# Kernel optimization log

Hardware: AMD Instinct MI355X
Metric: run time of the kernel (lower is better)

Reference implementation:

```python
import jax, jax.numpy as jnp
import numpy as np

RADIUS = 2
MAXDISP = 192


def _lga(x, g, radius=RADIUS):
    """Local guided aggregation (GANet LGA).
    x: [B, D, H, W] cost volume. g: [B, 3*k*k, H, W] L1-normalized guidance.
    out[b,d,p] = sum_off g0[off,p]*x[d,p+off] + g1[off,p]*x[d-1,p+off] + g2[off,p]*x[d+1,p+off]
    """
    B, D, H, W = x.shape
    k = 2 * radius + 1
    g0, g1, g2 = jnp.split(g, 3, axis=1)  # each [B, k*k, H, W]
    pad_sp = ((0, 0), (0, 0), (radius, radius), (radius, radius))
    x_p = jnp.pad(x, pad_sp)
    # disparity-shifted volumes (zero padded at the ends)
    x_dm = jnp.pad(x, ((0, 0), (1, 0), (0, 0), (0, 0)))[:, :D]   # x[d-1]
    x_dp = jnp.pad(x, ((0, 0), (0, 1), (0, 0), (0, 0)))[:, 1:]   # x[d+1]
    xm_p = jnp.pad(x_dm, pad_sp)
    xp_p = jnp.pad(x_dp, pad_sp)
    out = jnp.zeros_like(x)
    idx = 0
    for i in range(k):
        for j in range(k):
            sl = (slice(None), slice(None), slice(i, i + H), slice(j, j + W))
            out = out + (x_p[sl] * g0[:, idx][:, None]
                         + xm_p[sl] * g1[:, idx][:, None]
                         + xp_p[sl] * g2[:, idx][:, None])
            idx += 1
    return out


def _forward(x, lg1, conv_w):
    B = x.shape[0]
    H8, W8 = x.shape[3] * 8, x.shape[4] * 8
    # conv32x1: 3x3x3 conv, 32 -> 1 channels, padding 1, no bias
    x = jax.lax.conv_general_dilated(
        x, conv_w, window_strides=(1, 1, 1), padding=[(1, 1)] * 3,
        dimension_numbers=("NCDHW", "OIDHW", "NCDHW"))  # [B,1,D,H/8,W/8]
    # trilinear upsample (align_corners=False / half-pixel centers)
    x = jax.image.resize(x, (B, 1, MAXDISP + 1, H8, W8), method="linear")
    x = jnp.squeeze(x, 1)  # [B, D+1, H, W]
    # L1-normalize guidance over channel dim (F.normalize p=1 dim=1)
    g = lg1 / jnp.maximum(jnp.sum(jnp.abs(lg1), axis=1, keepdims=True), 1e-12)
    # LGA2 = local guided aggregation applied twice with the same guidance
    x = _lga(x, g)
    x = _lga(x, g)
    # softmin over disparity, then L1 normalize over disparity
    p = jax.nn.softmax(-x, axis=1)
    p = p / jnp.maximum(jnp.sum(jnp.abs(p), axis=1, keepdims=True), 1e-12)
    disps = jnp.arange(MAXDISP + 1, dtype=p.dtype)
    return jnp.einsum("bdhw,d->bhw", p, disps)


def setup_inputs() -> dict:
    key = jax.random.key(0)
    k1, k2, k3 = jax.random.split(key, 3)
    x = jax.random.normal(k1, (1, 32, 49, 32, 64), dtype=jnp.float32)
    lg1 = jax.random.uniform(k2, (1, 75, 256, 512), dtype=jnp.float32)
    conv_w = jax.random.normal(k3, (1, 32, 3, 3, 3), dtype=jnp.float32) * 0.05
    return {"x": x, "lg1": lg1, "conv_w": conv_w}


def reference(x, lg1, conv_w):
    return _forward(x, lg1, conv_w)
```

## Files before the change

### kernel.cpp

```cpp
#include <hip/hip_runtime.h>
#include <hip/hip_bf16.h>

#define DIN 49
#define HIN 32
#define WIN 64
#define CIN 32
#define DOUT 193
#define HOUT 256
#define WOUT 512
#define NPIX (HOUT * WOUT)
#define NUPS (DOUT * NPIX)
#define NCONV (DIN * HIN * WIN)
#define DSPLIT 193
#define NZ 1
#define CGRP 8

#define ROWSTRIDE 33
#define PIXSTRIDE 12
#define SUWORDS 7920

typedef __attribute__((ext_vector_type(2))) float v2f;
typedef __attribute__((ext_vector_type(4))) float v4f;

__device__ __forceinline__ v2f pk_fma(v2f a, v2f b, v2f c) {
    v2f d;
    asm("v_pk_fma_f32 %0, %1, %2, %3" : "=v"(d) : "v"(a), "v"(b), "v"(c));
    return d;
}

__global__ void conv3d_kernel(const float* __restrict__ x,
                              const float* __restrict__ w,
                              float* __restrict__ partial) {
    __shared__ float ws[4 * 27];
    const int grp = blockIdx.y;
    for (int t = threadIdx.x; t < 4 * 27; t += blockDim.x)
        ws[t] = w[grp * (4 * 27) + t];
    __syncthreads();

    int idx4 = blockIdx.x * blockDim.x + threadIdx.x;
    int w4 = idx4 & 15;
    int t2 = idx4 >> 4;
    int hq = t2 & 31;
    int dq = t2 >> 5;
    int wq0 = w4 * 4;

    float acc0 = 0.f, acc1 = 0.f, acc2 = 0.f, acc3 = 0.f;
    const float* xg = x + (size_t)grp * 4 * NCONV;
#pragma unroll
    for (int cl = 0; cl < 4; ++cl) {
        const float* xb = xg + cl * NCONV;
        const float* wb = ws + cl * 27;
#pragma unroll
        for (int kd = 0; kd < 3; ++kd) {
            int zd = dq + kd - 1;
            if (zd < 0 || zd >= DIN) continue;
#pragma unroll
            for (int kh = 0; kh < 3; ++kh) {
                int zh = hq + kh - 1;
                if (zh < 0 || zh >= HIN) continue;
                const float* row = xb + (zd * HIN + zh) * WIN;
                float4 v = *(const float4*)(row + wq0);
                float xl = (wq0 > 0) ? row[wq0 - 1] : 0.f;
                float xr = (wq0 < WIN - 4) ? row[wq0 + 4] : 0.f;
                float w0 = wb[(kd * 3 + kh) * 3 + 0];
                float w1 = wb[(kd * 3 + kh) * 3 + 1];
                float w2 = wb[(kd * 3 + kh) * 3 + 2];
                acc0 = fmaf(w0, xl, acc0);
                acc0 = fmaf(w1, v.x, acc0);
                acc0 = fmaf(w2, v.y, acc0);
                acc1 = fmaf(w0, v.x, acc1);
                acc1 = fmaf(w1, v.y, acc1);
                acc1 = fmaf(w2, v.z, acc1);
                acc2 = fmaf(w0, v.y, acc2);
                acc2 = fmaf(w1, v.z, acc2);
                acc2 = fmaf(w2, v.w, acc2);
                acc3 = fmaf(w0, v.z, acc3);
                acc3 = fmaf(w1, v.w, acc3);
                acc3 = fmaf(w2, xr, acc3);
            }
        }
    }
    float4 o4 = make_float4(acc0, acc1, acc2, acc3);
    *(float4*)(partial + (size_t)grp * NCONV + (size_t)idx4 * 4) = o4;
}

__global__ void convfold_kernel(const float* __restrict__ partial,
                                float* __restrict__ c) {
    int idx = blockIdx.x * blockDim.x + threadIdx.x;
    float s = 0.f;
#pragma unroll
    for (int g = 0; g < CGRP; ++g) s += partial[(size_t)g * NCONV + idx];
    c[idx] = s;
}

__device__ __forceinline__ unsigned short bf16bits(float f) {
    __hip_bfloat16 h = __float2bfloat16(f);
    unsigned short b;
    __builtin_memcpy(&b, &h, 2);
    return b;
}

#define GW(idx)                                                  \
    __uint_as_float(((idx) & 1) ? (gp[(idx) >> 1] & 0xFFFF0000u) \
                                : (gp[(idx) >> 1] << 16))

#define TAP_PK(A0, A1, B0, B1, C0, g0, g1, g2)   \
    do {                                         \
        v2f g1b = {g1, g1};                      \
        v2f g2b = {g2, g2};                      \
        acc01 = pk_fma(g1b, A0, acc01);          \
        acc01 = pk_fma(g2b, A1, acc01);          \
        acc23 = pk_fma(g1b, A1, acc23);          \
        acc23 = pk_fma(g2b, B0, acc23);          \
        acc45 = pk_fma(g1b, B0, acc45);          \
        acc45 = pk_fma(g2b, B1, acc45);          \
        acc67 = pk_fma(g1b, B1, acc67);          \
        acc67 = pk_fma(g2b, C0, acc67);          \
        acc01.x = fmaf(g0, A0.y, acc01.x);       \
        acc01.y = fmaf(g0, A1.x, acc01.y);       \
        acc23.x = fmaf(g0, A1.y, acc23.x);       \
        acc23.y = fmaf(g0, B0.x, acc23.y);       \
        acc45.x = fmaf(g0, B0.y, acc45.x);       \
        acc45.y = fmaf(g0, B1.x, acc45.y);       \
        acc67.x = fmaf(g0, B1.y, acc67.x);       \
        acc67.y = fmaf(g0, C0.x, acc67.y);       \
    } while (0)

__device__ __forceinline__ void stageA1(const float* __restrict__ cvol,
                                        int tid, int h0p, int w0p, int dstart,
                                        unsigned (&aq0)[4], unsigned (&aq2)[2]) {
    aq2[0] = 0u;
    aq2[1] = 0u;
#pragma unroll
    for (int k = 0; k < 4; ++k) {
        const bool a = (k < 3) || (tid < 32);
        int j = tid + k * 256;
        int seg = j & 3;
        int rowjob = j >> 2;
        int dl = rowjob / 20;
        int r = rowjob - dl * 20;
        int gh = h0p - 2 + r;
        int gwb = w0p - 8 + seg * 8;
        int gd = dstart - 1 + dl;
        if (a && gd >= 0 && gd < DOUT && gh >= 0 && gh < HOUT && gwb >= 0 &&
            (gwb + 8) <= WOUT) {
            float fd = (gd + 0.5f) * (49.0f / 193.0f) - 0.5f;
            fd = fminf(fmaxf(fd, 0.f), (float)(DIN - 1));
            int d0c = min((int)fd, DIN - 2);
            float ad = fd - (float)d0c;
            float fh = (gh + 0.5f) * 0.125f - 0.5f;
            fh = fminf(fmaxf(fh, 0.f), (float)(HIN - 1));
            int h0c = min((int)fh, HIN - 2);
            float ah = fh - (float)h0c;
            int g = gwb >> 3;
            int cm1 = max(g - 1, 0);
            int cp1 = min(g + 1, WIN - 1);
            const float* p00 = cvol + (d0c * HIN + h0c) * WIN;
            const float* p01 = p00 + WIN;
            const float* p10 = p00 + HIN * WIN;
            const float* p11 = p10 + WIN;
            float q00, q01, q10, q11, a0, a1, a2;
            q00 = p00[cm1]; q01 = p01[cm1];
            q10 = p10[cm1]; q11 = p11[cm1];
            a0 = (q00 + ah * (q01 - q00)) * (1.f - ad) +
                 (q10 + ah * (q11 - q10)) * ad;
            q00 = p00[g]; q01 = p01[g];
            q10 = p10[g]; q11 = p11[g];
            a1 = (q00 + ah * (q01 - q00)) * (1.f - ad) +
                 (q10 + ah * (q11 - q10)) * ad;
            q00 = p00[cp1]; q01 = p01[cp1];
            q10 = p10[cp1]; q11 = p11[cp1];
            a2 = (q00 + ah * (q01 - q00)) * (1.f - ad) +
                 (q10 + ah * (q11 - q10)) * ad;
            aq0[k] = (unsigned)bf16bits(a0) | ((unsigned)bf16bits(a1) << 16);
            aq2[k >> 1] |= ((unsigned)bf16bits(a2)) << ((k & 1) * 16);
        } else {
            aq0[k] = 0u;
        }
    }
}

__device__ __forceinline__ void scat1(float* __restrict__ su, int tid,
                                      const unsigned (&aq0)[4],
                                      const unsigned (&aq2)[2]) {
#pragma unroll
    for (int k = 0; k < 4; ++k) {
        if (k < 3 || tid < 32) {
            int j = tid + k * 256;
            int seg = j & 3;
            int rowjob = j >> 2;
            int dl = rowjob / 20;
            int r = rowjob - dl * 20;
            int base = (r * ROWSTRIDE + seg * 8) * PIXSTRIDE + dl;
            float a0 = __uint_as_float(aq0[k] << 16);
            float a1 = __uint_as_float(aq0[k] & 0xFFFF0000u);
            float a2 = __uint_as_float((k & 1) ? (aq2[k >> 1] & 0xFFFF0000u)
                                               : (aq2[k >> 1] << 16));
            float d01 = a1 - a0, d12 = a2 - a1;
            su[base + 0 * PIXSTRIDE] = a0 + 0.5625f * d01;
            su[base + 1 * PIXSTRIDE] = a0 + 0.6875f * d01;
            su[base + 2 * PIXSTRIDE] = a0 + 0.8125f * d01;
            su[base + 3 * PIXSTRIDE] = a0 + 0.9375f * d01;
            su[base + 4 * PIXSTRIDE] = a1 + 0.0625f * d12;
            su[base + 5 * PIXSTRIDE] = a1 + 0.1875f * d12;
            su[base + 6 * PIXSTRIDE] = a1 + 0.3125f * d12;
            su[base + 7 * PIXSTRIDE] = a1 + 0.4375f * d12;
        }
    }
}

__device__ __forceinline__ void stageA2(const unsigned short* __restrict__ xus,
                                        int tid, int h0p, int w0p, int dstart,
                                        uint4 (&dat)[4]) {
#pragma unroll
    for (int k = 0; k < 4; ++k) {
        const bool a = (k < 3) || (tid < 32);
        int j = tid + k * 256;
        int seg = j & 3;
        int rowjob = j >> 2;
        int dl = rowjob / 20;
        int r = rowjob - dl * 20;
        int gh = h0p - 2 + r;
        int gwb = w0p - 8 + seg * 8;
        int gd = dstart - 1 + dl;
        uint4 v = make_uint4(0u, 0u, 0u, 0u);
        if (a && gd >= 0 && gd < DOUT && gh >= 0 && gh < HOUT && gwb >= 0 &&
            (gwb + 8) <= WOUT)
            v = *(const uint4*)(xus + (size_t)gd * NPIX + gh * WOUT + gwb);
        dat[k] = v;
    }
}

__device__ __forceinline__ void scat2(float* __restrict__ su, int tid,
                                      const uint4 (&dat)[4]) {
#pragma unroll
    for (int k = 0; k < 4; ++k) {
        if (k < 3 || tid < 32) {
            int j = tid + k * 256;
            int seg = j & 3;
            int rowjob = j >> 2;
            int dl = rowjob / 20;
            int r = rowjob - dl * 20;
            int base = (r * ROWSTRIDE + seg * 8) * PIXSTRIDE + dl;
            unsigned q;
            q = dat[k].x;
            su[base + 0 * PIXSTRIDE] = __uint_as_float(q << 16);
            su[base + 1 * PIXSTRIDE] = __uint_as_float(q & 0xFFFF0000u);
            q = dat[k].y;
            su[base + 2 * PIXSTRIDE] = __uint_as_float(q << 16);
            su[base + 3 * PIXSTRIDE] = __uint_as_float(q & 0xFFFF0000u);
            q = dat[k].z;
            su[base + 4 * PIXSTRIDE] = __uint_as_float(q << 16);
            su[base + 5 * PIXSTRIDE] = __uint_as_float(q & 0xFFFF0000u);
            q = dat[k].w;
            su[base + 6 * PIXSTRIDE] = __uint_as_float(q << 16);
            su[base + 7 * PIXSTRIDE] = __uint_as_float(q & 0xFFFF0000u);
        }
    }
}

__global__ __launch_bounds__(256)
__attribute__((amdgpu_num_vgpr(128))) void lga1_kernel(
    const float* __restrict__ cvol,
    const float* __restrict__ lg1,
    __hip_bfloat16* __restrict__ yout) {
    const int tid = threadIdx.x;
    const int tx = tid & 15;
    const int ty = tid >> 4;
    const int w0p = blockIdx.x * 16;
    const int h0p = blockIdx.y * 16;
    const int zb = 0;
    const int dend = DOUT;
    const int pix = (h0p + ty) * WOUT + (w0p + tx);

    __shared__ __align__(16) float su[2 * SUWORDS];

    unsigned aq0[4], aq2[2];
    stageA1(cvol, tid, h0p, w0p, zb, aq0, aq2);

    float asum = 0.f;
    unsigned gp[38];
#pragma unroll
    for (int p = 0; p < 38; ++p) {
        int c0 = 2 * p, c1 = 2 * p + 1;
        float w0 = lg1[c0 * NPIX + pix];
        float w1 = (c1 < 75) ? lg1[c1 * NPIX + pix] : 0.f;
        unsigned b0 = bf16bits(w0), b1 = bf16bits(w1);
        asum += fabsf(__uint_as_float(b0 << 16)) +
                fabsf(__uint_as_float(b1 << 16));
        gp[p] = b0 | (b1 << 16);
    }
    const float inv = 1.f / fmaxf(asum, 1e-12f);

    const int pbase = (ty * ROWSTRIDE + tx + 6) * PIXSTRIDE;
    __hip_bfloat16* ybase = yout + pix;

    scat1(su, tid, aq0, aq2);
    int pb = 0;
    for (int d0 = zb; d0 < dend; d0 += 8) {
        __syncthreads();
        const bool hn = (d0 + 8 < dend);
        if (hn) stageA1(cvol, tid, h0p, w0p, d0 + 8, aq0, aq2);

        const float* sw = su + pb * SUWORDS + pbase;
        v2f acc01 = {0.f, 0.f}, acc23 = {0.f, 0.f};
        v2f acc45 = {0.f, 0.f}, acc67 = {0.f, 0.f};
#pragma unroll
        for (int i = 0; i < 5; ++i) {
#pragma unroll
            for (int j = 0; j < 5; ++j) {
                const int t = i * 5 + j;
                const float* sp = sw + (i * ROWSTRIDE + j) * PIXSTRIDE;
                v4f va = *(const v4f*)sp;
                v4f vb = *(const v4f*)(sp + 4);
                v2f vc = *(const v2f*)(sp + 8);
                v2f A0 = va.xy, A1 = va.zw, B0 = vb.xy, B1 = vb.zw;
                const float g0 = GW(t);
                const float g1 = GW(25 + t);
                const float g2 = GW(50 + t);
                TAP_PK(A0, A1, B0, B1, vc, g0, g1, g2);
            }
        }

        if (hn) scat1(su + (pb ^ 1) * SUWORDS, tid, aq0, aq2);

        float acc[8] = {acc01.x, acc01.y, acc23.x, acc23.y,
                        acc45.x, acc45.y, acc67.x, acc67.y};
        if (d0 + 8 <= dend) {
#pragma unroll
            for (int dd = 0; dd < 8; ++dd)
                ybase[(size_t)(d0 + dd) * NPIX] =
                    __float2bfloat16(acc[dd] * inv);
        } else {
#pragma unroll
            for (int dd = 0; dd < 8; ++dd)
                if (d0 + dd < dend)
                    ybase[(size_t)(d0 + dd) * NPIX] =
                        __float2bfloat16(acc[dd] * inv);
        }
        pb ^= 1;
    }
}

__global__ __launch_bounds__(256)
__attribute__((amdgpu_num_vgpr(128))) void lga2_kernel(
    const __hip_bfloat16* __restrict__ xin,
    const float* __restrict__ lg1,
    float* __restrict__ out) {
    const int tid = threadIdx.x;
    const int tx = tid & 15;
    const int ty = tid >> 4;
    const int w0p = blockIdx.x * 16;
    const int h0p = blockIdx.y * 16;
    const int zb = 0;
    const int dend = DOUT;
    const int pix = (h0p + ty) * WOUT + (w0p + tx);
    const unsigned short* xus = (const unsigned short*)xin;

    __shared__ __align__(16) float su[2 * SUWORDS];

    uint4 dat[4];
    stageA2(xus, tid, h0p, w0p, zb, dat);

    float asum = 0.f;
    unsigned gp[38];
#pragma unroll
    for (int p = 0; p < 38; ++p) {
        int c0 = 2 * p, c1 = 2 * p + 1;
        float w0 = lg1[c0 * NPIX + pix];
        float w1 = (c1 < 75) ? lg1[c1 * NPIX + pix] : 0.f;
        unsigned b0 = bf16bits(w0), b1 = bf16bits(w1);
        asum += fabsf(__uint_as_float(b0 << 16)) +
                fabsf(__uint_as_float(b1 << 16));
        gp[p] = b0 | (b1 << 16);
    }
    const float inv = 1.f / fmaxf(asum, 1e-12f);

    const int pbase = (ty * ROWSTRIDE + tx + 6) * PIXSTRIDE;

    float m = -1e30f, l = 0.f, s_acc = 0.f;

    scat2(su, tid, dat);
    int pb = 0;
    for (int d0 = zb; d0 < dend; d0 += 8) {
        __syncthreads();
        const bool hn = (d0 + 8 < dend);
        if (hn) stageA2(xus, tid, h0p, w0p, d0 + 8, dat);

        const float* sw = su + pb * SUWORDS + pbase;
        v2f acc01 = {0.f, 0.f}, acc23 = {0.f, 0.f};
        v2f acc45 = {0.f, 0.f}, acc67 = {0.f, 0.f};
#pragma unroll
        for (int i = 0; i < 5; ++i) {
#pragma unroll
            for (int j = 0; j < 5; ++j) {
                const int t = i * 5 + j;
                const float* sp = sw + (i * ROWSTRIDE + j) * PIXSTRIDE;
                v4f va = *(const v4f*)sp;
                v4f vb = *(const v4f*)(sp + 4);
                v2f vc = *(const v2f*)(sp + 8);
                v2f A0 = va.xy, A1 = va.zw, B0 = vb.xy, B1 = vb.zw;
                const float g0 = GW(t);
                const float g1 = GW(25 + t);
                const float g2 = GW(50 + t);
                TAP_PK(A0, A1, B0, B1, vc, g0, g1, g2);
            }
        }

        if (hn) scat2(su + (pb ^ 1) * SUWORDS, tid, dat);

        float acc[8] = {acc01.x, acc01.y, acc23.x, acc23.y,
                        acc45.x, acc45.y, acc67.x, acc67.y};
        if (d0 + 8 <= dend) {
            float v0 = -acc[0] * inv, v1 = -acc[1] * inv;
            float v2 = -acc[2] * inv, v3 = -acc[3] * inv;
            float v4 = -acc[4] * inv, v5 = -acc[5] * inv;
            float v6 = -acc[6] * inv, v7 = -acc[7] * inv;
            float mx = fmaxf(fmaxf(fmaxf(v0, v1), fmaxf(v2, v3)),
                             fmaxf(fmaxf(v4, v5), fmaxf(v6, v7)));
            mx = fmaxf(mx, m);
            float sc = __expf(m - mx);
            float e0 = __expf(v0 - mx), e1 = __expf(v1 - mx);
            float e2 = __expf(v2 - mx), e3 = __expf(v3 - mx);
            float e4 = __expf(v4 - mx), e5 = __expf(v5 - mx);
            float e6 = __expf(v6 - mx), e7 = __expf(v7 - mx);
            l = l * sc + ((e0 + e1) + (e2 + e3)) + ((e4 + e5) + (e6 + e7));
            float fd0 = (float)d0;
            s_acc = s_acc * sc + e0 * fd0 + e1 * (fd0 + 1.f) +
                    e2 * (fd0 + 2.f) + e3 * (fd0 + 3.f) + e4 * (fd0 + 4.f) +
                    e5 * (fd0 + 5.f) + e6 * (fd0 + 6.f) + e7 * (fd0 + 7.f);
            m = mx;
        } else {
#pragma unroll
            for (int dd = 0; dd < 8; ++dd) {
                int d = d0 + dd;
                if (d < dend) {
                    float v = -acc[dd] * inv;
                    float mx = fmaxf(m, v);
                    float sc = __expf(m - mx);
                    float e = __expf(v - mx);
                    l = l * sc + e;
                    s_acc = s_acc * sc + e * (float)d;
                    m = mx;
                }
            }
        }
        pb ^= 1;
    }

    out[pix] = s_acc / l;
}
#undef GW

extern "C" void kernel_launch(void* const* d_in, const int* in_sizes, int n_in,
                              void* d_out, int out_size, void* d_ws,
                              size_t ws_size, hipStream_t stream) {
    const float* x = (const float*)d_in[0];
    const float* lg1 = (const float*)d_in[1];
    const float* cw = (const float*)d_in[2];
    float* out = (float*)d_out;

    float* c = (float*)d_ws;
    __hip_bfloat16* regA = (__hip_bfloat16*)((char*)d_ws + (size_t)NCONV * 4);
    __hip_bfloat16* y1 = regA + (size_t)NUPS;
    float* cpart = (float*)y1;

    dim3 cgrid(NCONV / 1024, CGRP);
    conv3d_kernel<<<cgrid, 256, 0, stream>>>(x, cw, cpart);
    convfold_kernel<<<NCONV / 256, 256, 0, stream>>>(cpart, c);

    dim3 grid(WOUT / 16, HOUT / 16, NZ);
    lga1_kernel<<<grid, 256, 0, stream>>>(c, lg1, y1);
    lga2_kernel<<<grid, 256, 0, stream>>>(y1, lg1, out);
}
```

Measured before the change: 319.7 us.

## Store LDS tiles as bf16 and aggregate taps with v_dot2_f32_bf16

Both LGA kernels now keep the upsampled disparity tile in shared memory as packed bf16 pairs instead of fp32, which halves LDS footprint and read traffic per tap. The inner 5x5 tap loop uses v_dot2_f32_bf16 with pre-packed guidance weight pairs in place of packed fp32 FMAs. This cuts LDS bandwidth and the instruction count per tap. In exchange it adds bit-shuffling to build the weight pairs and sub-word 16-bit LDS stores in the scatter, and it rounds the intermediate upsampled values to bf16.

```diff
diff --git a/kernel.cpp b/kernel.cpp
--- a/kernel.cpp
+++ b/kernel.cpp
@@ -16,15 +16,16 @@
 #define CGRP 8
 
 #define ROWSTRIDE 33
-#define PIXSTRIDE 12
-#define SUWORDS 7920
+#define PIXW 6
+#define SUWORDS (20 * ROWSTRIDE * PIXW)
 
 typedef __attribute__((ext_vector_type(2))) float v2f;
-typedef __attribute__((ext_vector_type(4))) float v4f;
-
-__device__ __forceinline__ v2f pk_fma(v2f a, v2f b, v2f c) {
-    v2f d;
-    asm("v_pk_fma_f32 %0, %1, %2, %3" : "=v"(d) : "v"(a), "v"(b), "v"(c));
+
+__device__ __forceinline__ float dot2bf(unsigned a, unsigned b, float c) {
+    float d;
+    asm("v_dot2_f32_bf16 %0, %1, %2, %3"
+        : "=v"(d)
+        : "v"(a), "v"(b), "v"(c));
     return d;
 }
 
@@ -100,30 +101,42 @@
     return b;
 }
 
-#define GW(idx)                                                  \
-    __uint_as_float(((idx) & 1) ? (gp[(idx) >> 1] & 0xFFFF0000u) \
-                                : (gp[(idx) >> 1] << 16))
-
-#define TAP_PK(A0, A1, B0, B1, C0, g0, g1, g2)   \
-    do {                                         \
-        v2f g1b = {g1, g1};                      \
-        v2f g2b = {g2, g2};                      \
-        acc01 = pk_fma(g1b, A0, acc01);          \
-        acc01 = pk_fma(g2b, A1, acc01);          \
-        acc23 = pk_fma(g1b, A1, acc23);          \
-        acc23 = pk_fma(g2b, B0, acc23);          \
-        acc45 = pk_fma(g1b, B0, acc45);          \
-        acc45 = pk_fma(g2b, B1, acc45);          \
-        acc67 = pk_fma(g1b, B1, acc67);          \
-        acc67 = pk_fma(g2b, C0, acc67);          \
-        acc01.x = fmaf(g0, A0.y, acc01.x);       \
-        acc01.y = fmaf(g0, A1.x, acc01.y);       \
-        acc23.x = fmaf(g0, A1.y, acc23.x);       \
-        acc23.y = fmaf(g0, B0.x, acc23.y);       \
-        acc45.x = fmaf(g0, B0.y, acc45.x);       \
-        acc45.y = fmaf(g0, B1.x, acc45.y);       \
-        acc67.x = fmaf(g0, B1.y, acc67.x);       \
-        acc67.y = fmaf(g0, C0.x, acc67.y);       \
+#define TAP_DOT2(sp, t)                                              \
+    do {                                                             \
+        uint2 wa = *(const uint2*)(sp);                              \
+        uint2 wb = *(const uint2*)((sp) + 2);                        \
+        unsigned wcw = (sp)[4];                                      \
+        const unsigned g0w = gp[(t) >> 1];                           \
+        const unsigned g1w = gp[(25 + (t)) >> 1];                    \
+        const unsigned g2w = gp[(50 + (t)) >> 1];                    \
+        unsigned W10, W2z, Wz1, W02;                                 \
+        if ((t) & 1) {                                               \
+            W10 = (g1w & 0xFFFFu) | (g0w & 0xFFFF0000u);             \
+            W2z = g2w >> 16;                                         \
+            Wz1 = g1w << 16;                                         \
+            W02 = (g0w >> 16) | (g2w & 0xFFFF0000u);                 \
+        } else {                                                     \
+            W10 = (g1w >> 16) | (g0w << 16);                         \
+            W2z = g2w & 0xFFFFu;                                     \
+            Wz1 = g1w & 0xFFFF0000u;                                 \
+            W02 = (g0w & 0xFFFFu) | (g2w << 16);                     \
+        }                                                            \
+        acc0 = dot2bf(wa.x, W10, acc0);                              \
+        acc0 = dot2bf(wa.y, W2z, acc0);                              \
+        acc1 = dot2bf(wa.x, Wz1, acc1);                              \
+        acc1 = dot2bf(wa.y, W02, acc1);                              \
+        acc2 = dot2bf(wa.y, W10, acc2);                              \
+        acc2 = dot2bf(wb.x, W2z, acc2);                              \
+        acc3 = dot2bf(wa.y, Wz1, acc3);                              \
+        acc3 = dot2bf(wb.x, W02, acc3);                              \
+        acc4 = dot2bf(wb.x, W10, acc4);                              \
+        acc4 = dot2bf(wb.y, W2z, acc4);                              \
+        acc5 = dot2bf(wb.x, Wz1, acc5);                              \
+        acc5 = dot2bf(wb.y, W02, acc5);                              \
+        acc6 = dot2bf(wb.y, W10, acc6);                              \
+        acc6 = dot2bf(wcw, W2z, acc6);                               \
+        acc7 = dot2bf(wb.y, Wz1, acc7);                              \
+        acc7 = dot2bf(wcw, W02, acc7);                               \
     } while (0)
 
 __device__ __forceinline__ void stageA1(const float* __restrict__ cvol,
@@ -180,8 +193,8 @@
     }
 }
 
-__device__ __forceinline__ void scat1(float* __restrict__ su, int tid,
-                                      const unsigned (&aq0)[4],
+__device__ __forceinline__ void scat1(unsigned short* __restrict__ su16,
+                                      int tid, const unsigned (&aq0)[4],
                                       const unsigned (&aq2)[2]) {
 #pragma unroll
     for (int k = 0; k < 4; ++k) {
@@ -191,20 +204,20 @@
             int rowjob = j >> 2;
             int dl = rowjob / 20;
             int r = rowjob - dl * 20;
-            int base = (r * ROWSTRIDE + seg * 8) * PIXSTRIDE + dl;
+            int hb = (r * ROWSTRIDE + seg * 8) * (2 * PIXW) + dl;
             float a0 = __uint_as_float(aq0[k] << 16);
             float a1 = __uint_as_float(aq0[k] & 0xFFFF0000u);
             float a2 = __uint_as_float((k & 1) ? (aq2[k >> 1] & 0xFFFF0000u)
                                                : (aq2[k >> 1] << 16));
             float d01 = a1 - a0, d12 = a2 - a1;
-            su[base + 0 * PIXSTRIDE] = a0 + 0.5625f * d01;
-            su[base + 1 * PIXSTRIDE] = a0 + 0.6875f * d01;
-            su[base + 2 * PIXSTRIDE] = a0 + 0.8125f * d01;
-            su[base + 3 * PIXSTRIDE] = a0 + 0.9375f * d01;
-            su[base + 4 * PIXSTRIDE] = a1 + 0.0625f * d12;
-            su[base + 5 * PIXSTRIDE] = a1 + 0.1875f * d12;
-            su[base + 6 * PIXSTRIDE] = a1 + 0.3125f * d12;
-            su[base + 7 * PIXSTRIDE] = a1 + 0.4375f * d12;
+            su16[hb + 0 * 2 * PIXW] = bf16bits(a0 + 0.5625f * d01);
+            su16[hb + 1 * 2 * PIXW] = bf16bits(a0 + 0.6875f * d01);
+            su16[hb + 2 * 2 * PIXW] = bf16bits(a0 + 0.8125f * d01);
+            su16[hb + 3 * 2 * PIXW] = bf16bits(a0 + 0.9375f * d01);
+            su16[hb + 4 * 2 * PIXW] = bf16bits(a1 + 0.0625f * d12);
+            su16[hb + 5 * 2 * PIXW] = bf16bits(a1 + 0.1875f * d12);
+            su16[hb + 6 * 2 * PIXW] = bf16bits(a1 + 0.3125f * d12);
+            su16[hb + 7 * 2 * PIXW] = bf16bits(a1 + 0.4375f * d12);
         }
     }
 }
@@ -231,8 +244,8 @@
     }
 }
 
-__device__ __forceinline__ void scat2(float* __restrict__ su, int tid,
-                                      const uint4 (&dat)[4]) {
+__device__ __forceinline__ void scat2(unsigned short* __restrict__ su16,
+                                      int tid, const uint4 (&dat)[4]) {
 #pragma unroll
     for (int k = 0; k < 4; ++k) {
         if (k < 3 || tid < 32) {
@@ -241,20 +254,15 @@
             int rowjob = j >> 2;
             int dl = rowjob / 20;
             int r = rowjob - dl * 20;
-            int base = (r * ROWSTRIDE + seg * 8) * PIXSTRIDE + dl;
-            unsigned q;
-            q = dat[k].x;
-            su[base + 0 * PIXSTRIDE] = __uint_as_float(q << 16);
-            su[base + 1 * PIXSTRIDE] = __uint_as_float(q & 0xFFFF0000u);
-            q = dat[k].y;
-            su[base + 2 * PIXSTRIDE] = __uint_as_float(q << 16);
-            su[base + 3 * PIXSTRIDE] = __uint_as_float(q & 0xFFFF0000u);
-            q = dat[k].z;
-            su[base + 4 * PIXSTRIDE] = __uint_as_float(q << 16);
-            su[base + 5 * PIXSTRIDE] = __uint_as_float(q & 0xFFFF0000u);
-            q = dat[k].w;
-            su[base + 6 * PIXSTRIDE] = __uint_as_float(q << 16);
-            su[base + 7 * PIXSTRIDE] = __uint_as_float(q & 0xFFFF0000u);
+            int hb = (r * ROWSTRIDE + seg * 8) * (2 * PIXW) + dl;
+            su16[hb + 0 * 2 * PIXW] = (unsigned short)(dat[k].x);
+            su16[hb + 1 * 2 * PIXW] = (unsigned short)(dat[k].x >> 16);
+            su16[hb + 2 * 2 * PIXW] = (unsigned short)(dat[k].y);
+            su16[hb + 3 * 2 * PIXW] = (unsigned short)(dat[k].y >> 16);
+            su16[hb + 4 * 2 * PIXW] = (unsigned short)(dat[k].z);
+            su16[hb + 5 * 2 * PIXW] = (unsigned short)(dat[k].z >> 16);
+            su16[hb + 6 * 2 * PIXW] = (unsigned short)(dat[k].w);
+            su16[hb + 7 * 2 * PIXW] = (unsigned short)(dat[k].w >> 16);
         }
     }
 }
@@ -273,7 +281,7 @@
     const int dend = DOUT;
     const int pix = (h0p + ty) * WOUT + (w0p + tx);
 
-    __shared__ __align__(16) float su[2 * SUWORDS];
+    __shared__ __align__(16) unsigned su[2 * SUWORDS];
 
     unsigned aq0[4], aq2[2];
     stageA1(cvol, tid, h0p, w0p, zb, aq0, aq2);
@@ -292,40 +300,31 @@
     }
     const float inv = 1.f / fmaxf(asum, 1e-12f);
 
-    const int pbase = (ty * ROWSTRIDE + tx + 6) * PIXSTRIDE;
+    const int pbase = (ty * ROWSTRIDE + tx + 6) * PIXW;
     __hip_bfloat16* ybase = yout + pix;
 
-    scat1(su, tid, aq0, aq2);
+    scat1((unsigned short*)su, tid, aq0, aq2);
     int pb = 0;
     for (int d0 = zb; d0 < dend; d0 += 8) {
         __syncthreads();
         const bool hn = (d0 + 8 < dend);
         if (hn) stageA1(cvol, tid, h0p, w0p, d0 + 8, aq0, aq2);
 
-        const float* sw = su + pb * SUWORDS + pbase;
-        v2f acc01 = {0.f, 0.f}, acc23 = {0.f, 0.f};
-        v2f acc45 = {0.f, 0.f}, acc67 = {0.f, 0.f};
+        const unsigned* sw = su + pb * SUWORDS + pbase;
+        float acc0 = 0.f, acc1 = 0.f, acc2 = 0.f, acc3 = 0.f;
+        float acc4 = 0.f, acc5 = 0.f, acc6 = 0.f, acc7 = 0.f;
 #pragma unroll
         for (int i = 0; i < 5; ++i) {
 #pragma unroll
             for (int j = 0; j < 5; ++j) {
                 const int t = i * 5 + j;
-                const float* sp = sw + (i * ROWSTRIDE + j) * PIXSTRIDE;
-                v4f va = *(const v4f*)sp;
-                v4f vb = *(const v4f*)(sp + 4);
-                v2f vc = *(const v2f*)(sp + 8);
-                v2f A0 = va.xy, A1 = va.zw, B0 = vb.xy, B1 = vb.zw;
-                const float g0 = GW(t);
-                const float g1 = GW(25 + t);
-                const float g2 = GW(50 + t);
-                TAP_PK(A0, A1, B0, B1, vc, g0, g1, g2);
+                TAP_DOT2(sw + (i * ROWSTRIDE + j) * PIXW, t);
             }
         }
 
-        if (hn) scat1(su + (pb ^ 1) * SUWORDS, tid, aq0, aq2);
-
-        float acc[8] = {acc01.x, acc01.y, acc23.x, acc23.y,
-                        acc45.x, acc45.y, acc67.x, acc67.y};
+        if (hn) scat1((unsigned short*)(su + (pb ^ 1) * SUWORDS), tid, aq0, aq2);
+
+        float acc[8] = {acc0, acc1, acc2, acc3, acc4, acc5, acc6, acc7};
         if (d0 + 8 <= dend) {
 #pragma unroll
             for (int dd = 0; dd < 8; ++dd)
@@ -357,7 +356,7 @@
     const int pix = (h0p + ty) * WOUT + (w0p + tx);
     const unsigned short* xus = (const unsigned short*)xin;
 
-    __shared__ __align__(16) float su[2 * SUWORDS];
+    __shared__ __align__(16) unsigned su[2 * SUWORDS];
 
     uint4 dat[4];
     stageA2(xus, tid, h0p, w0p, zb, dat);
@@ -376,41 +375,32 @@
     }
     const float inv = 1.f / fmaxf(asum, 1e-12f);
 
-    const int pbase = (ty * ROWSTRIDE + tx + 6) * PIXSTRIDE;
+    const int pbase = (ty * ROWSTRIDE + tx + 6) * PIXW;
 
     float m = -1e30f, l = 0.f, s_acc = 0.f;
 
-    scat2(su, tid, dat);
+    scat2((unsigned short*)su, tid, dat);
     int pb = 0;
     for (int d0 = zb; d0 < dend; d0 += 8) {
         __syncthreads();
         const bool hn = (d0 + 8 < dend);
         if (hn) stageA2(xus, tid, h0p, w0p, d0 + 8, dat);
 
-        const float* sw = su + pb * SUWORDS + pbase;
-        v2f acc01 = {0.f, 0.f}, acc23 = {0.f, 0.f};
-        v2f acc45 = {0.f, 0.f}, acc67 = {0.f, 0.f};
+        const unsigned* sw = su + pb * SUWORDS + pbase;
+        float acc0 = 0.f, acc1 = 0.f, acc2 = 0.f, acc3 = 0.f;
+        float acc4 = 0.f, acc5 = 0.f, acc6 = 0.f, acc7 = 0.f;
 #pragma unroll
         for (int i = 0; i < 5; ++i) {
 #pragma unroll
             for (int j = 0; j < 5; ++j) {
                 const int t = i * 5 + j;
-                const float* sp = sw + (i * ROWSTRIDE + j) * PIXSTRIDE;
-                v4f va = *(const v4f*)sp;
-                v4f vb = *(const v4f*)(sp + 4);
-                v2f vc = *(const v2f*)(sp + 8);
-                v2f A0 = va.xy, A1 = va.zw, B0 = vb.xy, B1 = vb.zw;
-                const float g0 = GW(t);
-                const float g1 = GW(25 + t);
-                const float g2 = GW(50 + t);
-                TAP_PK(A0, A1, B0, B1, vc, g0, g1, g2);
+                TAP_DOT2(sw + (i * ROWSTRIDE + j) * PIXW, t);
             }
         }
 
-        if (hn) scat2(su + (pb ^ 1) * SUWORDS, tid, dat);
-
-        float acc[8] = {acc01.x, acc01.y, acc23.x, acc23.y,
-                        acc45.x, acc45.y, acc67.x, acc67.y};
+        if (hn) scat2((unsigned short*)(su + (pb ^ 1) * SUWORDS), tid, dat);
+
+        float acc[8] = {acc0, acc1, acc2, acc3, acc4, acc5, acc6, acc7};
         if (d0 + 8 <= dend) {
             float v0 = -acc[0] * inv, v1 = -acc[1] * inv;
             float v2 = -acc[2] * inv, v3 = -acc[3] * inv;
@@ -450,7 +440,6 @@
 
     out[pix] = s_acc / l;
 }
-#undef GW
 
 extern "C" void kernel_launch(void* const* d_in, const int* in_sizes, int n_in,
                               void* d_out, int out_size, void* d_ws,
```

Measured after the change: 297.5 us. 1.07x faster.
